# Optimization experiments

Hardware: AMD Instinct MI355X
Metric: run time of the kernel (lower is better)

Reference implementation:

```python
import jax, jax.numpy as jnp
import numpy as np

N = 50000      # nodes
E = 800000     # edges (avg degree 16)
IN, H, C = 256, 128, 64
LPA_ITER = 10


def setup_inputs() -> dict:
    key = jax.random.key(0)
    ks = jax.random.split(key, 8)
    x = jax.random.normal(ks[0], (N, IN), dtype=jnp.float32)
    soft_labels = jax.random.uniform(ks[1], (N, C), dtype=jnp.float32)
    edge_index = jax.random.randint(ks[2], (2, E), 0, N, dtype=jnp.int64)
    edge_attr = jax.random.uniform(ks[3], (E,), dtype=jnp.float32)  # abs(edge_weights), positive
    W1 = jax.random.normal(ks[4], (IN, H), dtype=jnp.float32) * (1.0 / np.sqrt(IN))
    b1 = jnp.zeros((H,), dtype=jnp.float32)
    W2 = jax.random.normal(ks[5], (H, C), dtype=jnp.float32) * (1.0 / np.sqrt(H))
    b2 = jnp.zeros((C,), dtype=jnp.float32)
    return {"x": x, "soft_labels": soft_labels, "edge_index": edge_index,
            "edge_attr": edge_attr, "W1": W1, "b1": b1, "W2": W2, "b2": b2}


def reference(x, soft_labels, edge_index, edge_attr, W1, b1, W2, b2):
    row, col = edge_index[0], edge_index[1]
    # Row-normalize sparse adjacency: deg[i] = sum of edge values in row i,
    # value <- value / deg[row]  (deg^-1 with inf -> 0)
    deg = jax.ops.segment_sum(edge_attr, row, num_segments=N)
    deg_inv = jnp.where(deg > 0, 1.0 / deg, 0.0)
    val = edge_attr * deg_inv[row]  # [E]

    def spmm(m):
        # out[i] = sum_{(i,j) in E} A[i,j] * m[j]
        return jax.ops.segment_sum(val[:, None] * m[col], row, num_segments=N)

    # GCNConv(normalize=False): spmm(A, x @ W) + b ; dropout is identity in eval mode
    h = jax.nn.relu(spmm(x @ W1) + b1)
    out = spmm(h @ W2) + b2

    # Label propagation: lpa_iter sparse-dense spmm steps
    labels = soft_labels
    for _ in range(LPA_ITER):
        labels = spmm(labels)
    return out, labels
```

## Files before the change

### kernel.cpp

```cpp
#include <hip/hip_runtime.h>

#define NN 50000
#define EE 800000
#define FIN 256
#define FH 128
#define FC 64
#define LPA_ITERS 10
#define NBLK 196

typedef __attribute__((ext_vector_type(8))) short short8v;
typedef __attribute__((ext_vector_type(4))) float f32x4;

__device__ __forceinline__ int edge_at(const int* __restrict__ ei, int is32, int which, int e) {
    int idx = which * EE + e;
    return is32 ? ei[idx] : ei[2 * idx];
}

__global__ void detect_k(const unsigned int* __restrict__ w, int* __restrict__ flag) {
    int any = 0;
    for (int i = 1 + 2 * (int)threadIdx.x; i < 2048; i += 2 * (int)blockDim.x)
        if (w[i] != 0u) any = 1;
    if (any) atomicOr(flag, 1);
}

__device__ __forceinline__ unsigned short bf16_rne(float f) {
    unsigned u = __float_as_uint(f);
    return (unsigned short)((u + 0x7FFFu + ((u >> 16) & 1u)) >> 16);
}
__device__ __forceinline__ unsigned packbf2(float a, float b) {
    return (unsigned)bf16_rne(a) | ((unsigned)bf16_rne(b) << 16);
}

__global__ __launch_bounds__(256) void accum_k(const int* __restrict__ ei,
                                               const int* __restrict__ flag,
                                               int* __restrict__ cnt,
                                               int* __restrict__ slot) {
    int e = blockIdx.x * 256 + threadIdx.x;
    if (e >= EE) return;
    int is32 = *flag;
    int r = edge_at(ei, is32, 0, e);
    slot[e] = atomicAdd(&cnt[r], 1);
}

__global__ __launch_bounds__(256) void scan1_k(const int* __restrict__ cnt,
                                               int* __restrict__ start,
                                               int* __restrict__ bsum,
                                               int* __restrict__ blockhist) {
    __shared__ int wtot[4];
    __shared__ int hist[64];
    int t = threadIdx.x, blk = blockIdx.x;
    int i = blk * 256 + t;
    if (t < 64) hist[t] = 0;
    __syncthreads();
    int c = (i < NN) ? cnt[i] : 0;
    if (i < NN) atomicAdd(&hist[c < 63 ? c : 63], 1);
    int lane = t & 63, w = t >> 6;
    int s = c;
    for (int d = 1; d < 64; d <<= 1) {
        int u = __shfl_up(s, d, 64);
        if (lane >= d) s += u;
    }
    if (lane == 63) wtot[w] = s;
    __syncthreads();
    int woff = 0;
    for (int j = 0; j < 4; ++j)
        if (j < w) woff += wtot[j];
    int excl = s - c + woff;
    if (i < NN) start[i] = excl;
    if (t == 255) bsum[blk] = excl + c;
    if (t < 64) blockhist[t * NBLK + blk] = hist[t];
}

__global__ void scan2_k(int* __restrict__ bsum, int* __restrict__ blockhist) {
    __shared__ int wtot[4];
    __shared__ int btot[64];
    int t = threadIdx.x;
    int lane = t & 63, w = t >> 6;
    int v = (t < NBLK) ? bsum[t] : 0;
    int s = v;
    for (int d = 1; d < 64; d <<= 1) {
        int u = __shfl_up(s, d, 64);
        if (lane >= d) s += u;
    }
    if (lane == 63) wtot[w] = s;
    __syncthreads();
    int woff = 0;
    for (int j = 0; j < 4; ++j)
        if (j < w) woff += wtot[j];
    if (t < NBLK) bsum[t] = s - v + woff;
    if (t < 64) {
        int run = 0;
        for (int j = 0; j < NBLK; ++j) {
            int idx = t * NBLK + j;
            int tmp = blockhist[idx];
            blockhist[idx] = run;
            run += tmp;
        }
        btot[t] = run;
    }
    __syncthreads();
    if (t < 64) {
        int bv = btot[t];
        int bs = bv;
        for (int d = 1; d < 64; d <<= 1) {
            int u = __shfl_up(bs, d, 64);
            if (lane >= d) bs += u;
        }
        int base = bs - bv;
        for (int j = 0; j < NBLK; ++j) blockhist[t * NBLK + j] += base;
    }
}

__global__ __launch_bounds__(256) void finish_k(const int* __restrict__ cnt,
                                                int* __restrict__ start,
                                                const int* __restrict__ bsum,
                                                const int* __restrict__ blockhist,
                                                int* __restrict__ perm) {
    __shared__ int hist[64];
    int t = threadIdx.x, blk = blockIdx.x;
    int i = blk * 256 + t;
    if (t < 64) hist[t] = 0;
    __syncthreads();
    if (i < NN) {
        start[i] += bsum[blk];
        int c = cnt[i];
        int b = c < 63 ? c : 63;
        int rank = atomicAdd(&hist[b], 1);
        perm[blockhist[b * NBLK + blk] + rank] = i;
    }
}

__global__ __launch_bounds__(256) void scatter_k(const int* __restrict__ ei,
                                                 const int* __restrict__ flag,
                                                 const float* __restrict__ ea,
                                                 const int* __restrict__ start,
                                                 const int* __restrict__ slot,
                                                 uint2* __restrict__ csr) {
    int e = blockIdx.x * 256 + threadIdx.x;
    if (e >= EE) return;
    int is32 = *flag;
    int r = edge_at(ei, is32, 0, e);
    int c = edge_at(ei, is32, 1, e);
    csr[start[r] + slot[e]] = make_uint2((unsigned)c, __float_as_uint(ea[e]));
}

__global__ __launch_bounds__(256) void rowscale_k(const int* __restrict__ start,
                                                  const int* __restrict__ cnt,
                                                  const uint2* __restrict__ csr,
                                                  float* __restrict__ deginv) {
    int t = threadIdx.x;
    int r = blockIdx.x * 16 + (t >> 4);
    if (r >= NN) return;
    int fl = t & 15;
    int s = start[r], n = cnt[r];
    float sum = 0.f;
    for (int k = fl; k < n; k += 16) sum += __uint_as_float(csr[s + k].y);
    for (int d = 1; d < 16; d <<= 1) sum += __shfl_xor(sum, d, 16);
    if (fl == 0) deginv[r] = sum > 0.f ? 1.f / sum : 0.f;
}

__global__ __launch_bounds__(256) void wcvt_k(const float* __restrict__ W,
                                              short* __restrict__ hi,
                                              short* __restrict__ lo,
                                              int K, int N) {
    int i = blockIdx.x * 256 + threadIdx.x;
    if (i >= K * N) return;
    int k = i / N, n = i - k * N;
    float f = W[i];
    unsigned short h = bf16_rne(f);
    float hf = __uint_as_float((unsigned)h << 16);
    unsigned short l = bf16_rne(f - hf);
    hi[n * K + k] = (short)h;
    lo[n * K + k] = (short)l;
}

__global__ __launch_bounds__(256) void cast_k(const float* __restrict__ in,
                                              uint2* __restrict__ outb, int n4) {
    int i = blockIdx.x * 256 + threadIdx.x;
    if (i >= n4) return;
    float4 f = ((const float4*)in)[i];
    outb[i] = make_uint2(packbf2(f.x, f.y), packbf2(f.z, f.w));
}

template <int KDIM, int NCOLT, int NF, int ABF, int CBF>
__global__ __launch_bounds__(256) void mgemm2_k(const void* __restrict__ Ap,
                                                const short* __restrict__ Bhi0,
                                                const short* __restrict__ Blo0,
                                                void* __restrict__ Cp, int M) {
    static_assert((size_t)NF * 16 * 72 * 2 * 2 < 49152, "LDS must stay well under 64KB");
    __shared__ short bh[NF * 16][72];
    __shared__ short bl[NF * 16][72];
    const int NSTG = KDIM / 64;
    const int NCH = NF / 2;
    int t = threadIdx.x;
    int cb = blockIdx.y;
    const short* Bhi = Bhi0 + (size_t)cb * (NF * 16) * KDIM;
    const short* Blo = Blo0 + (size_t)cb * (NF * 16) * KDIM;
    int wid = t >> 6, l = t & 63, l15 = l & 15, lq = l >> 4;
    int row = blockIdx.x * 64 + wid * 16 + l15;
    bool rv = row < M;
    f32x4 acc[NF];
#pragma unroll
    for (int j = 0; j < NF; ++j) acc[j] = (f32x4){0.f, 0.f, 0.f, 0.f};

    short8v rh[NCH], rl[NCH];
    float4 af[2][4];
    short8v ab_[2][2];
#pragma unroll
    for (int b = 0; b < 2; ++b) {
        if (ABF) {
            ab_[b][0] = (short8v){0, 0, 0, 0, 0, 0, 0, 0};
            ab_[b][1] = (short8v){0, 0, 0, 0, 0, 0, 0, 0};
        } else {
#pragma unroll
            for (int q = 0; q < 4; ++q) af[b][q] = make_float4(0.f, 0.f, 0.f, 0.f);
        }
    }

    auto loadB = [&](int k0) {
#pragma unroll
        for (int j = 0; j < NCH; ++j) {
            int c = t + j * 256;
            int col = c >> 3;
            int kk = (c & 7) * 8;
            rh[j] = *(const short8v*)&Bhi[(size_t)col * KDIM + k0 + kk];
            rl[j] = *(const short8v*)&Blo[(size_t)col * KDIM + k0 + kk];
        }
    };
    auto loadA = [&](int k0, int buf) {
        if (!rv) return;
        if (ABF) {
            const short* A = (const short*)Ap;
            ab_[buf][0] = *(const short8v*)&A[(size_t)row * KDIM + k0 + 8 * lq];
            ab_[buf][1] = *(const short8v*)&A[(size_t)row * KDIM + k0 + 32 + 8 * lq];
        } else {
            const float* A = (const float*)Ap;
            const float4* p0 = (const float4*)&A[(size_t)row * KDIM + k0 + 8 * lq];
            af[buf][0] = p0[0];
            af[buf][1] = p0[1];
            const float4* p1 = (const float4*)&A[(size_t)row * KDIM + k0 + 32 + 8 * lq];
            af[buf][2] = p1[0];
            af[buf][3] = p1[1];
        }
    };

    loadB(0);
    loadA(0, 0);
#pragma unroll
    for (int sg = 0; sg < NSTG; ++sg) {
        __syncthreads();
#pragma unroll
        for (int j = 0; j < NCH; ++j) {
            int c = t + j * 256;
            int col = c >> 3;
            int kk = (c & 7) * 8;
            *(short8v*)&bh[col][kk] = rh[j];
            *(short8v*)&bl[col][kk] = rl[j];
        }
        __syncthreads();
        if (sg + 1 < NSTG) {
            loadB((sg + 1) * 64);
            loadA((sg + 1) * 64, (sg + 1) & 1);
        }
        int cbuf = sg & 1;
#pragma unroll
        for (int ks = 0; ks < 2; ++ks) {
            short8v ahi, alo;
            if (ABF) {
                ahi = ab_[cbuf][ks];
            } else {
                float av[8];
                float4 xa = af[cbuf][ks * 2], xb = af[cbuf][ks * 2 + 1];
                av[0] = xa.x; av[1] = xa.y; av[2] = xa.z; av[3] = xa.w;
                av[4] = xb.x; av[5] = xb.y; av[6] = xb.z; av[7] = xb.w;
#pragma unroll
                for (int e = 0; e < 8; ++e) {
                    unsigned short h = bf16_rne(av[e]);
                    float hf = __uint_as_float((unsigned)h << 16);
                    ahi[e] = (short)h;
                    alo[e] = (short)bf16_rne(av[e] - hf);
                }
            }
#pragma unroll
            for (int j = 0; j < NF; ++j) {
                int col = j * 16 + l15;
                short8v fh = *(const short8v*)&bh[col][ks * 32 + 8 * lq];
                short8v fo = *(const short8v*)&bl[col][ks * 32 + 8 * lq];
                acc[j] = __builtin_amdgcn_mfma_f32_16x16x32_bf16(ahi, fh, acc[j], 0, 0, 0);
                acc[j] = __builtin_amdgcn_mfma_f32_16x16x32_bf16(ahi, fo, acc[j], 0, 0, 0);
                if (!ABF)
                    acc[j] = __builtin_amdgcn_mfma_f32_16x16x32_bf16(alo, fh, acc[j], 0, 0, 0);
            }
        }
    }
    int rbase = blockIdx.x * 64 + wid * 16 + 4 * lq;
#pragma unroll
    for (int j = 0; j < NF; ++j) {
        int col = cb * (NF * 16) + j * 16 + l15;
#pragma unroll
        for (int e = 0; e < 4; ++e) {
            int r = rbase + e;
            if (r < M) {
                if (CBF)
                    ((unsigned short*)Cp)[(size_t)r * NCOLT + col] = bf16_rne(acc[j][e]);
                else
                    ((float*)Cp)[(size_t)r * NCOLT + col] = acc[j][e];
            }
        }
    }
}

__global__ __launch_bounds__(256) void spmm64_k(const int* __restrict__ perm,
                                                const int* __restrict__ start,
                                                const int* __restrict__ cnt,
                                                const float* __restrict__ deginv,
                                                const uint2* __restrict__ csr,
                                                const float* __restrict__ m,
                                                float* __restrict__ out,
                                                const float* __restrict__ bias) {
    int t = threadIdx.x;
    int p = blockIdx.x * 16 + (t >> 4);
    if (p >= NN) return;
    int r = perm[p];
    int fl = t & 15;
    const float4* m4 = (const float4*)m;
    float4 acc = make_float4(0.f, 0.f, 0.f, 0.f);
    int s = start[r], n = cnt[r];
    int k = 0;
    for (; k + 8 <= n; k += 8) {
        uint2 ev[8];
        float4 gv[8];
#pragma unroll
        for (int u = 0; u < 8; ++u) ev[u] = csr[s + k + u];
#pragma unroll
        for (int u = 0; u < 8; ++u) gv[u] = m4[(size_t)ev[u].x * 16 + fl];
#pragma unroll
        for (int u = 0; u < 8; ++u) {
            float v = __uint_as_float(ev[u].y);
            acc.x = fmaf(v, gv[u].x, acc.x); acc.y = fmaf(v, gv[u].y, acc.y);
            acc.z = fmaf(v, gv[u].z, acc.z); acc.w = fmaf(v, gv[u].w, acc.w);
        }
    }
    for (; k < n; ++k) {
        uint2 e = csr[s + k];
        float v = __uint_as_float(e.y);
        float4 g = m4[(size_t)e.x * 16 + fl];
        acc.x = fmaf(v, g.x, acc.x); acc.y = fmaf(v, g.y, acc.y);
        acc.z = fmaf(v, g.z, acc.z); acc.w = fmaf(v, g.w, acc.w);
    }
    float dv = deginv[r];
    acc.x *= dv; acc.y *= dv; acc.z *= dv; acc.w *= dv;
    if (bias) {
        float4 b = ((const float4*)bias)[fl];
        acc.x += b.x; acc.y += b.y; acc.z += b.z; acc.w += b.w;
    }
    ((float4*)out)[(size_t)r * 16 + fl] = acc;
}

__global__ __launch_bounds__(256) void spmm128b_k(const int* __restrict__ perm,
                                                  const int* __restrict__ start,
                                                  const int* __restrict__ cnt,
                                                  const float* __restrict__ deginv,
                                                  const uint2* __restrict__ csr,
                                                  const uint2* __restrict__ mb,
                                                  uint2* __restrict__ outb,
                                                  const float* __restrict__ bias) {
    int t = threadIdx.x;
    int p = blockIdx.x * 8 + (t >> 5);
    if (p >= NN) return;
    int r = perm[p];
    int fl = t & 31;
    float4 acc = make_float4(0.f, 0.f, 0.f, 0.f);
    int s = start[r], n = cnt[r];
    int k = 0;
    for (; k + 8 <= n; k += 8) {
        uint2 ev[8];
        uint2 gv[8];
#pragma unroll
        for (int u = 0; u < 8; ++u) ev[u] = csr[s + k + u];
#pragma unroll
        for (int u = 0; u < 8; ++u) gv[u] = mb[(size_t)ev[u].x * 32 + fl];
#pragma unroll
        for (int u = 0; u < 8; ++u) {
            float v = __uint_as_float(ev[u].y);
            acc.x = fmaf(v, __uint_as_float(gv[u].x << 16), acc.x);
            acc.y = fmaf(v, __uint_as_float(gv[u].x & 0xFFFF0000u), acc.y);
            acc.z = fmaf(v, __uint_as_float(gv[u].y << 16), acc.z);
            acc.w = fmaf(v, __uint_as_float(gv[u].y & 0xFFFF0000u), acc.w);
        }
    }
    for (; k < n; ++k) {
        uint2 e = csr[s + k];
        float v = __uint_as_float(e.y);
        uint2 g = mb[(size_t)e.x * 32 + fl];
        acc.x = fmaf(v, __uint_as_float(g.x << 16), acc.x);
        acc.y = fmaf(v, __uint_as_float(g.x & 0xFFFF0000u), acc.y);
        acc.z = fmaf(v, __uint_as_float(g.y << 16), acc.z);
        acc.w = fmaf(v, __uint_as_float(g.y & 0xFFFF0000u), acc.w);
    }
    float dv = deginv[r];
    float4 b = ((const float4*)bias)[fl];
    acc.x = fmaxf(fmaf(acc.x, dv, b.x), 0.f);
    acc.y = fmaxf(fmaf(acc.y, dv, b.y), 0.f);
    acc.z = fmaxf(fmaf(acc.z, dv, b.z), 0.f);
    acc.w = fmaxf(fmaf(acc.w, dv, b.w), 0.f);
    outb[(size_t)r * 32 + fl] = make_uint2(packbf2(acc.x, acc.y), packbf2(acc.z, acc.w));
}

__global__ __launch_bounds__(256) void spmm64b_k(const int* __restrict__ perm,
                                                 const int* __restrict__ start,
                                                 const int* __restrict__ cnt,
                                                 const float* __restrict__ deginv,
                                                 const uint2* __restrict__ csr,
                                                 const uint2* __restrict__ mb,
                                                 void* __restrict__ outp,
                                                 int f32out) {
    int t = threadIdx.x;
    int p = blockIdx.x * 16 + (t >> 4);
    if (p >= NN) return;
    int r = perm[p];
    int fl = t & 15;
    float4 acc = make_float4(0.f, 0.f, 0.f, 0.f);
    int s = start[r], n = cnt[r];
    int k = 0;
    for (; k + 8 <= n; k += 8) {
        uint2 ev[8];
        uint2 gv[8];
#pragma unroll
        for (int u = 0; u < 8; ++u) ev[u] = csr[s + k + u];
#pragma unroll
        for (int u = 0; u < 8; ++u) gv[u] = mb[(size_t)ev[u].x * 16 + fl];
#pragma unroll
        for (int u = 0; u < 8; ++u) {
            float v = __uint_as_float(ev[u].y);
            acc.x = fmaf(v, __uint_as_float(gv[u].x << 16), acc.x);
            acc.y = fmaf(v, __uint_as_float(gv[u].x & 0xFFFF0000u), acc.y);
            acc.z = fmaf(v, __uint_as_float(gv[u].y << 16), acc.z);
            acc.w = fmaf(v, __uint_as_float(gv[u].y & 0xFFFF0000u), acc.w);
        }
    }
    for (; k < n; ++k) {
        uint2 e = csr[s + k];
        float v = __uint_as_float(e.y);
        uint2 g = mb[(size_t)e.x * 16 + fl];
        acc.x = fmaf(v, __uint_as_float(g.x << 16), acc.x);
        acc.y = fmaf(v, __uint_as_float(g.x & 0xFFFF0000u), acc.y);
        acc.z = fmaf(v, __uint_as_float(g.y << 16), acc.z);
        acc.w = fmaf(v, __uint_as_float(g.y & 0xFFFF0000u), acc.w);
    }
    float dv = deginv[r];
    acc.x *= dv; acc.y *= dv; acc.z *= dv; acc.w *= dv;
    if (f32out) {
        ((float4*)outp)[(size_t)r * 16 + fl] = acc;
    } else {
        ((uint2*)outp)[(size_t)r * 16 + fl] =
            make_uint2(packbf2(acc.x, acc.y), packbf2(acc.z, acc.w));
    }
}

extern "C" void kernel_launch(void* const* d_in, const int* in_sizes, int n_in,
                              void* d_out, int out_size, void* d_ws, size_t ws_size,
                              hipStream_t stream) {
    const float* x    = (const float*)d_in[0];
    const float* soft = (const float*)d_in[1];
    const int*   ei   = (const int*)d_in[2];
    const float* ea   = (const float*)d_in[3];
    const float* W1   = (const float*)d_in[4];
    const float* b1   = (const float*)d_in[5];
    const float* W2   = (const float*)d_in[6];
    const float* b2   = (const float*)d_in[7];
    float* out  = (float*)d_out;
    float* labB = out + (size_t)NN * FC;

    char* ws = (char*)d_ws;
    size_t off = 0;
    auto alloc = [&](size_t b) { size_t o = off; off += (b + 255) & ~(size_t)255; return o; };
    size_t o_misc  = alloc(256);
    size_t o_cnt   = alloc((size_t)NN * 4);
    size_t zero_end = off;
    size_t o_start = alloc((size_t)NN * 4);
    size_t o_perm  = alloc((size_t)NN * 4);
    size_t o_dinv  = alloc((size_t)NN * 4);
    size_t o_bsum  = alloc((size_t)NBLK * 4);
    size_t o_bhist = alloc((size_t)64 * NBLK * 4);
    size_t o_slot  = alloc((size_t)EE * 4);
    size_t o_csr   = alloc((size_t)EE * 8);
    size_t o_w1h   = alloc((size_t)FIN * FH * 2);
    size_t o_w1l   = alloc((size_t)FIN * FH * 2);
    size_t o_w2h   = alloc((size_t)FH * FC * 2);
    size_t o_w2l   = alloc((size_t)FH * FC * 2);
    size_t o_t1    = alloc((size_t)NN * FH * 2);
    size_t o_h     = alloc((size_t)NN * FH * 2);
    size_t o_t2    = alloc((size_t)NN * FC * 4);
    size_t o_sbf   = alloc((size_t)NN * FC * 2);
    size_t o_lA    = alloc((size_t)NN * FC * 2);
    size_t o_lB    = alloc((size_t)NN * FC * 2);
    if (off > ws_size) return;

    int*   misc  = (int*)(ws + o_misc);
    int*   cnt   = (int*)(ws + o_cnt);
    int*   start = (int*)(ws + o_start);
    int*   perm  = (int*)(ws + o_perm);
    float* dinv  = (float*)(ws + o_dinv);
    int*   bsum  = (int*)(ws + o_bsum);
    int*   bhist = (int*)(ws + o_bhist);
    int*   slot  = (int*)(ws + o_slot);
    uint2* csr   = (uint2*)(ws + o_csr);
    short* w1h   = (short*)(ws + o_w1h);
    short* w1l   = (short*)(ws + o_w1l);
    short* w2h   = (short*)(ws + o_w2h);
    short* w2l   = (short*)(ws + o_w2l);
    void*  t1    = (void*)(ws + o_t1);
    uint2* h     = (uint2*)(ws + o_h);
    float* t2    = (float*)(ws + o_t2);
    uint2* sbf   = (uint2*)(ws + o_sbf);
    uint2* lA    = (uint2*)(ws + o_lA);
    uint2* lB    = (uint2*)(ws + o_lB);

    hipMemsetAsync(d_ws, 0, zero_end, stream);
    detect_k<<<1, 256, 0, stream>>>((const unsigned int*)ei, &misc[0]);
    accum_k<<<(EE + 255) / 256, 256, 0, stream>>>(ei, misc, cnt, slot);
    scan1_k<<<NBLK, 256, 0, stream>>>(cnt, start, bsum, bhist);
    scan2_k<<<1, 256, 0, stream>>>(bsum, bhist);
    finish_k<<<NBLK, 256, 0, stream>>>(cnt, start, bsum, bhist, perm);
    scatter_k<<<(EE + 255) / 256, 256, 0, stream>>>(ei, misc, ea, start, slot, csr);
    rowscale_k<<<(NN + 15) / 16, 256, 0, stream>>>(start, cnt, csr, dinv);
    wcvt_k<<<(FIN * FH + 255) / 256, 256, 0, stream>>>(W1, w1h, w1l, FIN, FH);
    wcvt_k<<<(FH * FC + 255) / 256, 256, 0, stream>>>(W2, w2h, w2l, FH, FC);
    cast_k<<<(NN * FC / 4 + 255) / 256, 256, 0, stream>>>(soft, sbf, NN * FC / 4);

    mgemm2_k<FIN, FH, 4, 0, 1><<<dim3((NN + 63) / 64, 2), 256, 0, stream>>>(
        x, w1h, w1l, t1, NN);
    spmm128b_k<<<(NN + 7) / 8, 256, 0, stream>>>(perm, start, cnt, dinv, csr,
                                                 (const uint2*)t1, h, b1);

    mgemm2_k<FH, FC, 4, 1, 0><<<dim3((NN + 63) / 64, 1), 256, 0, stream>>>(
        h, w2h, w2l, t2, NN);
    spmm64_k<<<(NN + 15) / 16, 256, 0, stream>>>(perm, start, cnt, dinv, csr, t2, out, b2);

    const uint2* src = sbf;
    uint2* dst = lA;
    for (int it = 0; it < LPA_ITERS; ++it) {
        int last = (it == LPA_ITERS - 1);
        spmm64b_k<<<(NN + 15) / 16, 256, 0, stream>>>(perm, start, cnt, dinv, csr, src,
                                                      last ? (void*)labB : (void*)dst, last);
        src = dst;
        dst = (dst == lA) ? lB : lA;
    }
}
```

Measured before the change: 370.9 us.

## Replace first-layer GEMM with register-prefetched, LDS-resident-B split-bf16 MFMA kernel

Adds a new GEMM kernel for x@W1 that loads the whole 32-column slice of the split hi/lo bf16 weights into XOR-swizzled LDS once. It then streams fp32 rows of A directly from global memory, with a three-slot register prefetch, converting them to hi/lo bf16 on the fly. Each wave computes two 16-row fragments using three MFMAs per product for near-fp32 accuracy. The goal is to remove the staged LDS pipeline of the old kernel and overlap A loads with compute. The cost is that x is re-read once for each of the four column blocks, and register pressure rises at 512 threads per block.

```diff
diff --git a/kernel.cpp b/kernel.cpp
--- a/kernel.cpp
+++ b/kernel.cpp
@@ -180,6 +180,118 @@
     if (i >= n4) return;
     float4 f = ((const float4*)in)[i];
     outb[i] = make_uint2(packbf2(f.x, f.y), packbf2(f.z, f.w));
+}
+
+template <int KDIM, int NCOLT, int NCOLB>
+__global__ __launch_bounds__(512) void pgemm_k(const float* __restrict__ A,
+                                               const short* __restrict__ Bhi0,
+                                               const short* __restrict__ Blo0,
+                                               unsigned short* __restrict__ Cb,
+                                               int M) {
+    static_assert((size_t)NCOLB * KDIM * 2 * 2 <= 32768, "LDS must stay <= 32KB");
+    const int NF = NCOLB / 16;
+    const int NSTEP = KDIM / 32;
+    __shared__ short bh[NCOLB * KDIM];
+    __shared__ short bl[NCOLB * KDIM];
+    int t = threadIdx.x;
+    int cb = blockIdx.y;
+    const short* Bh = Bhi0 + (size_t)cb * NCOLB * KDIM;
+    const short* Bl = Blo0 + (size_t)cb * NCOLB * KDIM;
+
+    const int CHK = NCOLB * KDIM / 8;
+#pragma unroll
+    for (int it = 0; it < CHK / 512; ++it) {
+        int c = it * 512 + t;
+        int col = c / (KDIM / 8);
+        int kk = (c - col * (KDIM / 8)) * 8;
+        int e = col * KDIM + kk;
+        int sidx = e ^ ((col & 7) << 3);
+        *(short8v*)&bh[sidx] = *(const short8v*)&Bh[e];
+        *(short8v*)&bl[sidx] = *(const short8v*)&Bl[e];
+    }
+    __syncthreads();
+
+    int wid = t >> 6, l = t & 63, l15 = l & 15, lq = l >> 4;
+    int wbase = blockIdx.x * 256 + wid * 32;
+    int row0 = wbase + l15, row1 = wbase + 16 + l15;
+    bool rv0 = row0 < M, rv1 = row1 < M;
+
+    f32x4 acc[2][NF];
+#pragma unroll
+    for (int rf = 0; rf < 2; ++rf)
+#pragma unroll
+        for (int j = 0; j < NF; ++j) acc[rf][j] = (f32x4){0.f, 0.f, 0.f, 0.f};
+
+    float4 afr[3][2][2];
+#pragma unroll
+    for (int b = 0; b < 3; ++b)
+#pragma unroll
+        for (int rf = 0; rf < 2; ++rf)
+#pragma unroll
+            for (int q = 0; q < 2; ++q) afr[b][rf][q] = make_float4(0.f, 0.f, 0.f, 0.f);
+
+    auto loadA = [&](int s, int slot) {
+        if (rv0) {
+            const float4* p = (const float4*)&A[(size_t)row0 * KDIM + s * 32 + 8 * lq];
+            afr[slot][0][0] = p[0];
+            afr[slot][0][1] = p[1];
+        }
+        if (rv1) {
+            const float4* p = (const float4*)&A[(size_t)row1 * KDIM + s * 32 + 8 * lq];
+            afr[slot][1][0] = p[0];
+            afr[slot][1][1] = p[1];
+        }
+    };
+    auto cvtA = [&](int slot, int rf, short8v& ahi, short8v& alo) {
+        float av[8];
+        float4 xa = afr[slot][rf][0], xb = afr[slot][rf][1];
+        av[0] = xa.x; av[1] = xa.y; av[2] = xa.z; av[3] = xa.w;
+        av[4] = xb.x; av[5] = xb.y; av[6] = xb.z; av[7] = xb.w;
+#pragma unroll
+        for (int e = 0; e < 8; ++e) {
+            unsigned short hh = bf16_rne(av[e]);
+            float hf = __uint_as_float((unsigned)hh << 16);
+            ahi[e] = (short)hh;
+            alo[e] = (short)bf16_rne(av[e] - hf);
+        }
+    };
+
+    loadA(0, 0);
+    if (NSTEP > 1) loadA(1, 1);
+#pragma unroll
+    for (int k = 0; k < NSTEP; ++k) {
+        if (k + 2 < NSTEP) loadA(k + 2, (k + 2) % 3);
+        int cs = k % 3;
+        short8v ahi0, alo0, ahi1, alo1;
+        cvtA(cs, 0, ahi0, alo0);
+        cvtA(cs, 1, ahi1, alo1);
+#pragma unroll
+        for (int j = 0; j < NF; ++j) {
+            int col = j * 16 + l15;
+            int boff = (col * KDIM + k * 32 + 8 * lq) ^ ((col & 7) << 3);
+            short8v fh = *(const short8v*)&bh[boff];
+            short8v fo = *(const short8v*)&bl[boff];
+            acc[0][j] = __builtin_amdgcn_mfma_f32_16x16x32_bf16(ahi0, fh, acc[0][j], 0, 0, 0);
+            acc[0][j] = __builtin_amdgcn_mfma_f32_16x16x32_bf16(ahi0, fo, acc[0][j], 0, 0, 0);
+            acc[0][j] = __builtin_amdgcn_mfma_f32_16x16x32_bf16(alo0, fh, acc[0][j], 0, 0, 0);
+            acc[1][j] = __builtin_amdgcn_mfma_f32_16x16x32_bf16(ahi1, fh, acc[1][j], 0, 0, 0);
+            acc[1][j] = __builtin_amdgcn_mfma_f32_16x16x32_bf16(ahi1, fo, acc[1][j], 0, 0, 0);
+            acc[1][j] = __builtin_amdgcn_mfma_f32_16x16x32_bf16(alo1, fh, acc[1][j], 0, 0, 0);
+        }
+    }
+
+#pragma unroll
+    for (int rf = 0; rf < 2; ++rf) {
+        int rb = wbase + rf * 16 + 4 * lq;
+#pragma unroll
+        for (int j = 0; j < NF; ++j)
+#pragma unroll
+            for (int e = 0; e < 4; ++e) {
+                int r = rb + e;
+                if (r < M)
+                    Cb[(size_t)r * NCOLT + cb * NCOLB + j * 16 + l15] = bf16_rne(acc[rf][j][e]);
+            }
+    }
 }
 
 template <int KDIM, int NCOLT, int NF, int ABF, int CBF>
@@ -529,8 +641,8 @@
     wcvt_k<<<(FH * FC + 255) / 256, 256, 0, stream>>>(W2, w2h, w2l, FH, FC);
     cast_k<<<(NN * FC / 4 + 255) / 256, 256, 0, stream>>>(soft, sbf, NN * FC / 4);
 
-    mgemm2_k<FIN, FH, 4, 0, 1><<<dim3((NN + 63) / 64, 2), 256, 0, stream>>>(
-        x, w1h, w1l, t1, NN);
+    pgemm_k<FIN, FH, 32><<<dim3((NN + 255) / 256, FH / 32), 512, 0, stream>>>(
+        x, w1h, w1l, (unsigned short*)t1, NN);
     spmm128b_k<<<(NN + 7) / 8, 256, 0, stream>>>(perm, start, cnt, dinv, csr,
                                                  (const uint2*)t1, h, b1);
 
```

Measured after the change: 387.7 us. +4.5%, slower.

## Co-schedule first four LPA iterations with GCN GEMM/SpMM stages in fused launches

Applied to the files above, without the earlier changes.

Merges each GCN stage (GEMM1, SpMM128, GEMM2, SpMM64) with one independent label-propagation iteration into a single launch, dispatching by block index. The intent is to fill idle CUs and tail gaps of the GCN kernels with LPA work and to cut four kernel launches. The cost is heterogeneous blocks sharing one kernel, so the fused kernel gets the larger register and LDS footprint of the GEMM path, which may lower occupancy for the SpMM blocks.

```diff
diff --git a/kernel.cpp b/kernel.cpp
--- a/kernel.cpp
+++ b/kernel.cpp
@@ -7,6 +7,9 @@
 #define FC 64
 #define LPA_ITERS 10
 #define NBLK 196
+#define G1X 782
+#define SPB 3125
+#define SP128B 6250
 
 typedef __attribute__((ext_vector_type(8))) short short8v;
 typedef __attribute__((ext_vector_type(4))) float f32x4;
@@ -182,22 +185,23 @@
     outb[i] = make_uint2(packbf2(f.x, f.y), packbf2(f.z, f.w));
 }
 
+
 template <int KDIM, int NCOLT, int NF, int ABF, int CBF>
-__global__ __launch_bounds__(256) void mgemm2_k(const void* __restrict__ Ap,
-                                                const short* __restrict__ Bhi0,
-                                                const short* __restrict__ Blo0,
-                                                void* __restrict__ Cp, int M) {
+__device__ __forceinline__ void mgemm2_body(int bx, int cb,
+                                            const void* __restrict__ Ap,
+                                            const short* __restrict__ Bhi0,
+                                            const short* __restrict__ Blo0,
+                                            void* __restrict__ Cp, int M) {
     static_assert((size_t)NF * 16 * 72 * 2 * 2 < 49152, "LDS must stay well under 64KB");
     __shared__ short bh[NF * 16][72];
     __shared__ short bl[NF * 16][72];
     const int NSTG = KDIM / 64;
     const int NCH = NF / 2;
     int t = threadIdx.x;
-    int cb = blockIdx.y;
     const short* Bhi = Bhi0 + (size_t)cb * (NF * 16) * KDIM;
     const short* Blo = Blo0 + (size_t)cb * (NF * 16) * KDIM;
     int wid = t >> 6, l = t & 63, l15 = l & 15, lq = l >> 4;
-    int row = blockIdx.x * 64 + wid * 16 + l15;
+    int row = bx * 64 + wid * 16 + l15;
     bool rv = row < M;
     f32x4 acc[NF];
 #pragma unroll
@@ -293,7 +297,7 @@
             }
         }
     }
-    int rbase = blockIdx.x * 64 + wid * 16 + 4 * lq;
+    int rbase = bx * 64 + wid * 16 + 4 * lq;
 #pragma unroll
     for (int j = 0; j < NF; ++j) {
         int col = cb * (NF * 16) + j * 16 + l15;
@@ -310,16 +314,16 @@
     }
 }
 
-__global__ __launch_bounds__(256) void spmm64_k(const int* __restrict__ perm,
-                                                const int* __restrict__ start,
-                                                const int* __restrict__ cnt,
-                                                const float* __restrict__ deginv,
-                                                const uint2* __restrict__ csr,
-                                                const float* __restrict__ m,
-                                                float* __restrict__ out,
-                                                const float* __restrict__ bias) {
+__device__ __forceinline__ void spmm64f_body(int pb, const int* __restrict__ perm,
+                                             const int* __restrict__ start,
+                                             const int* __restrict__ cnt,
+                                             const float* __restrict__ deginv,
+                                             const uint2* __restrict__ csr,
+                                             const float* __restrict__ m,
+                                             float* __restrict__ out,
+                                             const float* __restrict__ bias) {
     int t = threadIdx.x;
-    int p = blockIdx.x * 16 + (t >> 4);
+    int p = pb * 16 + (t >> 4);
     if (p >= NN) return;
     int r = perm[p];
     int fl = t & 15;
@@ -350,23 +354,21 @@
     }
     float dv = deginv[r];
     acc.x *= dv; acc.y *= dv; acc.z *= dv; acc.w *= dv;
-    if (bias) {
-        float4 b = ((const float4*)bias)[fl];
-        acc.x += b.x; acc.y += b.y; acc.z += b.z; acc.w += b.w;
-    }
+    float4 b = ((const float4*)bias)[fl];
+    acc.x += b.x; acc.y += b.y; acc.z += b.z; acc.w += b.w;
     ((float4*)out)[(size_t)r * 16 + fl] = acc;
 }
 
-__global__ __launch_bounds__(256) void spmm128b_k(const int* __restrict__ perm,
-                                                  const int* __restrict__ start,
-                                                  const int* __restrict__ cnt,
-                                                  const float* __restrict__ deginv,
-                                                  const uint2* __restrict__ csr,
-                                                  const uint2* __restrict__ mb,
-                                                  uint2* __restrict__ outb,
-                                                  const float* __restrict__ bias) {
+__device__ __forceinline__ void spmm128b_body(int pb, const int* __restrict__ perm,
+                                              const int* __restrict__ start,
+                                              const int* __restrict__ cnt,
+                                              const float* __restrict__ deginv,
+                                              const uint2* __restrict__ csr,
+                                              const uint2* __restrict__ mb,
+                                              uint2* __restrict__ outb,
+                                              const float* __restrict__ bias) {
     int t = threadIdx.x;
-    int p = blockIdx.x * 8 + (t >> 5);
+    int p = pb * 8 + (t >> 5);
     if (p >= NN) return;
     int r = perm[p];
     int fl = t & 31;
@@ -407,16 +409,15 @@
     outb[(size_t)r * 32 + fl] = make_uint2(packbf2(acc.x, acc.y), packbf2(acc.z, acc.w));
 }
 
-__global__ __launch_bounds__(256) void spmm64b_k(const int* __restrict__ perm,
-                                                 const int* __restrict__ start,
-                                                 const int* __restrict__ cnt,
-                                                 const float* __restrict__ deginv,
-                                                 const uint2* __restrict__ csr,
-                                                 const uint2* __restrict__ mb,
-                                                 void* __restrict__ outp,
-                                                 int f32out) {
+__device__ __forceinline__ void spmm64b_body(int pb, const int* __restrict__ perm,
+                                             const int* __restrict__ start,
+                                             const int* __restrict__ cnt,
+                                             const float* __restrict__ deginv,
+                                             const uint2* __restrict__ csr,
+                                             const uint2* __restrict__ mb,
+                                             void* __restrict__ outp, int f32out) {
     int t = threadIdx.x;
-    int p = blockIdx.x * 16 + (t >> 4);
+    int p = pb * 16 + (t >> 4);
     if (p >= NN) return;
     int r = perm[p];
     int fl = t & 15;
@@ -456,6 +457,88 @@
         ((uint2*)outp)[(size_t)r * 16 + fl] =
             make_uint2(packbf2(acc.x, acc.y), packbf2(acc.z, acc.w));
     }
+}
+
+
+__global__ __launch_bounds__(256) void f1_k(const float* __restrict__ x,
+                                            const short* __restrict__ w1h,
+                                            const short* __restrict__ w1l,
+                                            unsigned short* __restrict__ t1,
+                                            const int* __restrict__ perm,
+                                            const int* __restrict__ start,
+                                            const int* __restrict__ cnt,
+                                            const float* __restrict__ dinv,
+                                            const uint2* __restrict__ csr,
+                                            const uint2* __restrict__ sbf,
+                                            uint2* __restrict__ lA) {
+    int b = blockIdx.x;
+    if (b < 2 * G1X)
+        mgemm2_body<FIN, FH, 4, 0, 1>(b % G1X, b / G1X, x, w1h, w1l, t1, NN);
+    else
+        spmm64b_body(b - 2 * G1X, perm, start, cnt, dinv, csr, sbf, lA, 0);
+}
+
+__global__ __launch_bounds__(256) void f2_k(const int* __restrict__ perm,
+                                            const int* __restrict__ start,
+                                            const int* __restrict__ cnt,
+                                            const float* __restrict__ dinv,
+                                            const uint2* __restrict__ csr,
+                                            const uint2* __restrict__ t1,
+                                            uint2* __restrict__ h,
+                                            const float* __restrict__ b1,
+                                            const uint2* __restrict__ lA,
+                                            uint2* __restrict__ lB) {
+    int b = blockIdx.x;
+    if (b < SP128B)
+        spmm128b_body(b, perm, start, cnt, dinv, csr, t1, h, b1);
+    else
+        spmm64b_body(b - SP128B, perm, start, cnt, dinv, csr, lA, lB, 0);
+}
+
+__global__ __launch_bounds__(256) void f3_k(const unsigned short* __restrict__ h,
+                                            const short* __restrict__ w2h,
+                                            const short* __restrict__ w2l,
+                                            float* __restrict__ t2,
+                                            const int* __restrict__ perm,
+                                            const int* __restrict__ start,
+                                            const int* __restrict__ cnt,
+                                            const float* __restrict__ dinv,
+                                            const uint2* __restrict__ csr,
+                                            const uint2* __restrict__ lB,
+                                            uint2* __restrict__ lA) {
+    int b = blockIdx.x;
+    if (b < G1X)
+        mgemm2_body<FH, FC, 4, 1, 0>(b, 0, h, w2h, w2l, t2, NN);
+    else
+        spmm64b_body(b - G1X, perm, start, cnt, dinv, csr, lB, lA, 0);
+}
+
+__global__ __launch_bounds__(256) void f4_k(const int* __restrict__ perm,
+                                            const int* __restrict__ start,
+                                            const int* __restrict__ cnt,
+                                            const float* __restrict__ dinv,
+                                            const uint2* __restrict__ csr,
+                                            const float* __restrict__ t2,
+                                            float* __restrict__ out,
+                                            const float* __restrict__ b2,
+                                            const uint2* __restrict__ lA,
+                                            uint2* __restrict__ lB) {
+    int b = blockIdx.x;
+    if (b < SPB)
+        spmm64f_body(b, perm, start, cnt, dinv, csr, t2, out, b2);
+    else
+        spmm64b_body(b - SPB, perm, start, cnt, dinv, csr, lA, lB, 0);
+}
+
+__global__ __launch_bounds__(256) void spmm64b_k(const int* __restrict__ perm,
+                                                 const int* __restrict__ start,
+                                                 const int* __restrict__ cnt,
+                                                 const float* __restrict__ deginv,
+                                                 const uint2* __restrict__ csr,
+                                                 const uint2* __restrict__ mb,
+                                                 void* __restrict__ outp,
+                                                 int f32out) {
+    spmm64b_body(blockIdx.x, perm, start, cnt, deginv, csr, mb, outp, f32out);
 }
 
 extern "C" void kernel_launch(void* const* d_in, const int* in_sizes, int n_in,
@@ -510,7 +593,7 @@
     short* w1l   = (short*)(ws + o_w1l);
     short* w2h   = (short*)(ws + o_w2h);
     short* w2l   = (short*)(ws + o_w2l);
-    void*  t1    = (void*)(ws + o_t1);
+    unsigned short* t1 = (unsigned short*)(ws + o_t1);
     uint2* h     = (uint2*)(ws + o_h);
     float* t2    = (float*)(ws + o_t2);
     uint2* sbf   = (uint2*)(ws + o_sbf);
@@ -529,21 +612,21 @@
     wcvt_k<<<(FH * FC + 255) / 256, 256, 0, stream>>>(W2, w2h, w2l, FH, FC);
     cast_k<<<(NN * FC / 4 + 255) / 256, 256, 0, stream>>>(soft, sbf, NN * FC / 4);
 
-    mgemm2_k<FIN, FH, 4, 0, 1><<<dim3((NN + 63) / 64, 2), 256, 0, stream>>>(
-        x, w1h, w1l, t1, NN);
-    spmm128b_k<<<(NN + 7) / 8, 256, 0, stream>>>(perm, start, cnt, dinv, csr,
-                                                 (const uint2*)t1, h, b1);
-
-    mgemm2_k<FH, FC, 4, 1, 0><<<dim3((NN + 63) / 64, 1), 256, 0, stream>>>(
-        h, w2h, w2l, t2, NN);
-    spmm64_k<<<(NN + 15) / 16, 256, 0, stream>>>(perm, start, cnt, dinv, csr, t2, out, b2);
-
-    const uint2* src = sbf;
+    f1_k<<<2 * G1X + SPB, 256, 0, stream>>>(x, w1h, w1l, t1, perm, start, cnt, dinv,
+                                            csr, sbf, lA);
+    f2_k<<<SP128B + SPB, 256, 0, stream>>>(perm, start, cnt, dinv, csr,
+                                           (const uint2*)t1, h, b1, lA, lB);
+    f3_k<<<G1X + SPB, 256, 0, stream>>>((const unsigned short*)h, w2h, w2l, t2,
+                                        perm, start, cnt, dinv, csr, lB, lA);
+    f4_k<<<SPB + SPB, 256, 0, stream>>>(perm, start, cnt, dinv, csr, t2, out, b2,
+                                        lA, lB);
+
+    const uint2* src = lB;
     uint2* dst = lA;
-    for (int it = 0; it < LPA_ITERS; ++it) {
+    for (int it = 4; it < LPA_ITERS; ++it) {
         int last = (it == LPA_ITERS - 1);
-        spmm64b_k<<<(NN + 15) / 16, 256, 0, stream>>>(perm, start, cnt, dinv, csr, src,
-                                                      last ? (void*)labB : (void*)dst, last);
+        spmm64b_k<<<SPB, 256, 0, stream>>>(perm, start, cnt, dinv, csr, src,
+                                           last ? (void*)labB : (void*)dst, last);
         src = dst;
         dst = (dst == lA) ? lB : lA;
     }
```

New measurement: 358.9 us. 3.2% less time.
